# Optimization experiments

Hardware: AMD Instinct MI355X
Metric: run time of the kernel (lower is better)

The kernel has to match this reference:

```python
import jax, jax.numpy as jnp
import numpy as np

H = 1024      # hidden_size
NH = 16       # num_attention_heads
HD = H // NH  # head_size
DF = 4096     # ff intermediate
EPS = 1e-5


def layer_norm(x, g, b):
    mu = jnp.mean(x, axis=-1, keepdims=True)
    var = jnp.var(x, axis=-1, keepdims=True)
    return (x - mu) * jax.lax.rsqrt(var + EPS) * g + b


def setup_inputs() -> dict:
    key = jax.random.key(0)
    ks = jax.random.split(key, 4)
    s = 0.02
    return {
        "x": jax.random.normal(ks[0], (2, 2048, H), dtype=jnp.float32),
        "w_qkv": jax.random.normal(ks[1], (H, 3 * H), dtype=jnp.float32) * s,
        "ln1_g": jnp.ones((H,), jnp.float32),
        "ln1_b": jnp.zeros((H,), jnp.float32),
        "w1": jax.random.normal(ks[2], (H, DF), dtype=jnp.float32) * s,
        "b1": jnp.zeros((DF,), jnp.float32),
        "w2": jax.random.normal(ks[3], (DF, H), dtype=jnp.float32) * s,
        "b2": jnp.zeros((H,), jnp.float32),
        "ln2_g": jnp.ones((H,), jnp.float32),
        "ln2_b": jnp.zeros((H,), jnp.float32),
    }


def reference(x, w_qkv, ln1_g, ln1_b, w1, b1, w2, b2, ln2_g, ln2_b):
    b, s, h = x.shape
    # --- MHSelfAttention (naive) ---
    qkv = x @ w_qkv                                   # [b, s, 3h]
    qkv = qkv.reshape(b, s, 3, NH, HD)
    q, k, v = (jnp.moveaxis(qkv, 2, 0)                # [3, b, s, nh, hd]
               .transpose(0, 1, 3, 2, 4))             # [3, b, nh, s, hd]
    # NOTE: faithful quirk — scaled by sqrt(hidden_size), not head_size
    scores = jnp.einsum('bnqd,bnkd->bnqk', q, k) / jnp.sqrt(jnp.float32(h))
    probs = jax.nn.softmax(scores, axis=-1)
    ctx = jnp.einsum('bnqk,bnkd->bnqd', probs, v)     # [b, nh, s, hd]
    attn_out = ctx.transpose(0, 2, 1, 3).reshape(b, s, h)
    # post-norm residual (dropout = identity in eval)
    x = x + layer_norm(attn_out, ln1_g, ln1_b)
    # --- FFN ---
    ff = jax.nn.relu(x @ w1 + b1) @ w2 + b2
    x = x + layer_norm(ff, ln2_g, ln2_b)
    return x
```

## Files before the change

kernel.cpp:

```cpp
#include <hip/hip_runtime.h>


typedef unsigned short u16;
typedef unsigned int u32;
typedef __bf16 bf16x8 __attribute__((ext_vector_type(8)));
typedef float f32x4 __attribute__((ext_vector_type(4)));
typedef float f32x16 __attribute__((ext_vector_type(16)));
typedef u32 u32x4 __attribute__((ext_vector_type(4)));
typedef u16 u16x4 __attribute__((ext_vector_type(4)));

__device__ __forceinline__ u16 f2b(float f) {
  u32 u = __builtin_bit_cast(u32, f);
  u += 0x7fffu + ((u >> 16) & 1u);
  return (u16)(u >> 16);
}
__device__ __forceinline__ float b2f(u16 u) {
  return __builtin_bit_cast(float, (u32)u << 16);
}

__device__ __forceinline__ u32 cvtpk(float lo, float hi) {
  u32 r;
  asm("v_cvt_pk_bf16_f32 %0, %1, %2" : "=v"(r) : "v"(lo), "v"(hi));
  return r;
}

__device__ __forceinline__ void gld_lds16(const u16* g, u16* l) {
  __builtin_amdgcn_global_load_lds(
      (const __attribute__((address_space(1))) u32*)g,
      (__attribute__((address_space(3))) u32*)l, 16, 0, 0);
}

__global__ __launch_bounds__(256) void convert_bf16_kernel(
    const float* __restrict__ in, u16* __restrict__ out) {
  const int idx = blockIdx.x * 256 + threadIdx.x;
  float4 v = ((const float4*)in)[idx];
  u16x4 o = { f2b(v.x), f2b(v.y), f2b(v.z), f2b(v.w) };
  ((u16x4*)out)[idx] = o;
}

__global__ __launch_bounds__(256) void transpose_bf16_kernel(
    const float* __restrict__ in, u16* __restrict__ out, int R, int C) {
  __shared__ float tile[32][33];
  const int cb = blockIdx.x * 32, rb = blockIdx.y * 32;
  const int c = threadIdx.x & 31;
  const int r0 = threadIdx.x >> 5;
#pragma unroll
  for (int rr = 0; rr < 32; rr += 8)
    tile[r0 + rr][c] = in[(size_t)(rb + r0 + rr) * C + cb + c];
  __syncthreads();
#pragma unroll
  for (int rr = 0; rr < 32; rr += 8)
    out[(size_t)(cb + r0 + rr) * R + rb + c] = f2b(tile[c][r0 + rr]);
}

__global__ __launch_bounds__(256) void transpose_v_kernel(
    const u16* __restrict__ qkv, u16* __restrict__ vt) {
  __shared__ u16 t[64][70];
  const int bh = blockIdx.x, st = blockIdx.y;
  const int b = bh >> 4, nh = bh & 15;
  const int s0 = st * 64;
  const int r = threadIdx.x >> 3, c = (threadIdx.x & 7) << 3;
  const u16* src = qkv + (size_t)(b * 2048 + s0) * 3072 + 2048 + nh * 64;
#pragma unroll
  for (int rr = 0; rr < 64; rr += 32)
    *(u32x4*)&t[r + rr][c] = *(const u32x4*)(src + (size_t)(r + rr) * 3072 + c);
  __syncthreads();
  u16* dst = vt + ((size_t)bh * 64) * 2048 + s0;
#pragma unroll
  for (int rr = 0; rr < 64; rr += 32) {
    const int d = r + rr;
    u16 tmp[8];
#pragma unroll
    for (int j = 0; j < 8; ++j) tmp[j] = t[c + j][d];
    *(u32x4*)(dst + (size_t)d * 2048 + c) = *(u32x4*)tmp;
  }
}

#define GTILE(T, BUF, T2, VM)                                                 \
  {                                                                           \
    const u16(*Ab)[32] = As[BUF];                                             \
    const u16(*Bb)[32] = Bs[BUF];                                             \
    bf16x8 af[4], bf[4];                                                      \
    _Pragma("unroll") for (int nr = 0; nr < 4; ++nr)                          \
        bf[nr] = *(const bf16x8*)&Bb[wn * 64 + nr * 16 + l16][cRd];           \
    _Pragma("unroll") for (int mr = 0; mr < 4; ++mr)                          \
        af[mr] = *(const bf16x8*)&Ab[wm * 128 + mr * 16 + l16][cRd];          \
    if ((T2) >= 0) {                                                          \
      gld_lds16(Ag + (size_t)(T2) * 32,         &As[(T2) & 3][w * 16][0]);    \
      gld_lds16(Ag + rstep + (size_t)(T2) * 32, &As[(T2) & 3][128 + w * 16][0]);\
    }                                                                         \
    __builtin_amdgcn_sched_barrier(0);                                        \
    __builtin_amdgcn_s_barrier();                                             \
    asm volatile("s_waitcnt lgkmcnt(0)" ::: "memory");                        \
    __builtin_amdgcn_sched_barrier(0);                                        \
    __builtin_amdgcn_s_setprio(1);                                            \
    _Pragma("unroll") for (int mr = 0; mr < 4; ++mr)                          \
        _Pragma("unroll") for (int nr = 0; nr < 4; ++nr)                      \
            acc[mr][nr] = __builtin_amdgcn_mfma_f32_16x16x32_bf16(            \
                af[mr], bf[nr], acc[mr][nr], 0, 0, 0);                        \
    __builtin_amdgcn_s_setprio(0);                                            \
    __builtin_amdgcn_s_barrier();                                             \
    _Pragma("unroll") for (int mr = 0; mr < 4; ++mr)                          \
        af[mr] = *(const bf16x8*)&Ab[wm * 128 + 64 + mr * 16 + l16][cRd];     \
    if ((T2) >= 0) {                                                          \
      gld_lds16(Bg + (size_t)(T2) * 32,         &Bs[(T2) & 3][w * 16][0]);    \
      gld_lds16(Bg + rstep + (size_t)(T2) * 32, &Bs[(T2) & 3][128 + w * 16][0]);\
    }                                                                         \
    __builtin_amdgcn_sched_barrier(0);                                        \
    __builtin_amdgcn_s_barrier();                                             \
    asm volatile("s_waitcnt lgkmcnt(0)" ::: "memory");                        \
    __builtin_amdgcn_sched_barrier(0);                                        \
    __builtin_amdgcn_s_setprio(1);                                            \
    _Pragma("unroll") for (int mr = 0; mr < 4; ++mr)                          \
        _Pragma("unroll") for (int nr = 0; nr < 4; ++nr)                      \
            acc[4 + mr][nr] = __builtin_amdgcn_mfma_f32_16x16x32_bf16(        \
                af[mr], bf[nr], acc[4 + mr][nr], 0, 0, 0);                    \
    __builtin_amdgcn_s_setprio(0);                                            \
    if ((VM) == 4) asm volatile("s_waitcnt vmcnt(4)" ::: "memory");           \
    else if ((VM) == 0) asm volatile("s_waitcnt vmcnt(0)" ::: "memory");      \
    __builtin_amdgcn_s_barrier();                                             \
  }

__global__ __launch_bounds__(512) void gemm256_kernel(
    const u16* __restrict__ A, const u16* __restrict__ Bt,
    const float* __restrict__ bias, u16* __restrict__ Cb,
    int M, int N, int K, int relu,
    u16* __restrict__ Cb1, u16* __restrict__ Cb2, u16* __restrict__ Cb3) {
  const int nN = N >> 8;
  const int lin = (blockIdx.x & 7) * ((int)gridDim.x >> 3) + (blockIdx.x >> 3);
  const int m0 = (lin / nN) << 8;
  const int n0 = (lin % nN) << 8;
  const int z = blockIdx.y;
  if (z == 1) Cb = Cb1; else if (z == 2) Cb = Cb2; else if (z == 3) Cb = Cb3;

  const int tid = threadIdx.x;
  const int w = tid >> 6, lane = tid & 63;
  const int quad = lane >> 4, l16 = lane & 15;
  const int wm = w >> 2, wn = w & 3;

  __shared__ u16 As[4][256][32];
  __shared__ u16 Bs[4][256][32];

  f32x4 acc[8][4];
#pragma unroll
  for (int i = 0; i < 8; ++i)
#pragma unroll
    for (int j = 0; j < 4; ++j) acc[i][j] = {0.f, 0.f, 0.f, 0.f};

  const int srow = lane >> 2;
  const int scol = (((lane & 3) ^ (srow & 3)) << 3);
  const u16* Ag = A + (size_t)(m0 + w * 16 + srow) * K + (size_t)z * 1024 + scol;
  const u16* Bg = Bt + (size_t)(n0 + w * 16 + srow) * K + (size_t)z * 1024 + scol;
  const size_t rstep = (size_t)128 * K;

  const int cRd = ((quad ^ (l16 & 3)) << 3);

  gld_lds16(Ag,              &As[0][w * 16][0]);
  gld_lds16(Ag + rstep,      &As[0][128 + w * 16][0]);
  gld_lds16(Bg,              &Bs[0][w * 16][0]);
  gld_lds16(Bg + rstep,      &Bs[0][128 + w * 16][0]);
  gld_lds16(Ag + 32,         &As[1][w * 16][0]);
  gld_lds16(Ag + rstep + 32, &As[1][128 + w * 16][0]);
  gld_lds16(Bg + 32,         &Bs[1][w * 16][0]);
  gld_lds16(Bg + rstep + 32, &Bs[1][128 + w * 16][0]);
  asm volatile("s_waitcnt vmcnt(4)" ::: "memory");
  __builtin_amdgcn_s_barrier();

  for (int tt = 0; tt < 7; ++tt) {
    const int t = tt * 4;
    GTILE(t + 0, 0, t + 2, 4)
    GTILE(t + 1, 1, t + 3, 4)
    GTILE(t + 2, 2, t + 4, 4)
    GTILE(t + 3, 3, t + 5, 4)
  }
  GTILE(28, 0, 30, 4)
  GTILE(29, 1, 31, 4)
  GTILE(30, 2, -1, 0)
  GTILE(31, 3, -1, -1)

#pragma unroll
  for (int mr = 0; mr < 8; ++mr) {
    const int row = m0 + wm * 128 + mr * 16 + quad * 4;
#pragma unroll
    for (int nr = 0; nr < 4; ++nr) {
      const int col = n0 + wn * 64 + nr * 16 + l16;
      const float bv = bias ? bias[col] : 0.f;
#pragma unroll
      for (int r = 0; r < 4; ++r) {
        float v = acc[mr][nr][r] + bv;
        if (relu) v = fmaxf(v, 0.f);
        Cb[(size_t)(row + r) * N + col] = f2b(v);
      }
    }
  }
}

__global__ __launch_bounds__(256, 4) void attn_kernel(
    const u16* __restrict__ qkv, const u16* __restrict__ vt,
    float* __restrict__ Op0, float* __restrict__ Op1,
    float* __restrict__ lpart) {
  const int bh = blockIdx.x;
  const int qt = blockIdx.y;
  const int kz = blockIdx.z;
  const int b = bh >> 4, nh = bh & 15;
  const int tid = threadIdx.x;
  const int w = tid >> 6, lane = tid & 63;
  const int l32 = lane & 31, hi = lane >> 5;
  const float c2 = 0.04508422f;

  __shared__ u16 KS[64][64];
  __shared__ u16 VS[64][64];

  const size_t rs = 3072;
  const u16* qbase = qkv + (size_t)b * 2048 * rs + nh * 64;
  const u16* kbase = qbase + 1024;
  const u16* vbase = vt + (size_t)bh * 64 * 2048;
  const int q0 = qt * 128;
  const int k0beg = kz * 1024;

  bf16x8 aq[4];
  {
    const u16* qrow = qbase + (size_t)(q0 + w * 32 + l32) * rs + hi * 8;
#pragma unroll
    for (int ds = 0; ds < 4; ++ds) {
      u32x4 v = *(const u32x4*)(qrow + ds * 16);
      u16 ti[8], to[8];
      *(u32x4*)ti = v;
#pragma unroll
      for (int j = 0; j < 8; ++j) to[j] = f2b(b2f(ti[j]) * c2);
      u32x4 pk = *(u32x4*)to;
      aq[ds] = __builtin_bit_cast(bf16x8, pk);
    }
  }

  f32x16 Oacc[2];
#pragma unroll
  for (int dn = 0; dn < 2; ++dn)
#pragma unroll
    for (int i = 0; i < 16; ++i) Oacc[dn][i] = 0.f;
  float ls[4] = {0.f, 0.f, 0.f, 0.f};

  const int srow = lane >> 3;
  const int scol = ((lane & 7) ^ srow) << 3;

#pragma unroll 1
  for (int t = 0; t < 16; ++t) {
    const int k0 = k0beg + t * 64;
    __syncthreads();
    gld_lds16(kbase + (size_t)(k0 + w * 16 + srow) * rs + scol,       &KS[w * 16][0]);
    gld_lds16(kbase + (size_t)(k0 + w * 16 + 8 + srow) * rs + scol,   &KS[w * 16 + 8][0]);
    gld_lds16(vbase + (size_t)(w * 16 + srow) * 2048 + k0 + scol,     &VS[w * 16][0]);
    gld_lds16(vbase + (size_t)(w * 16 + 8 + srow) * 2048 + k0 + scol, &VS[w * 16 + 8][0]);
    __syncthreads();

    f32x16 S[2];
#pragma unroll
    for (int jt = 0; jt < 2; ++jt)
#pragma unroll
      for (int i = 0; i < 16; ++i) S[jt][i] = 0.f;
#pragma unroll
    for (int jt = 0; jt < 2; ++jt) {
      const int krow = jt * 32 + l32;
#pragma unroll
      for (int ds = 0; ds < 4; ++ds) {
        bf16x8 kv = *(const bf16x8*)&KS[krow][((2 * ds + hi) ^ (krow & 7)) << 3];
        S[jt] = __builtin_amdgcn_mfma_f32_32x32x16_bf16(kv, aq[ds], S[jt], 0, 0, 0);
      }
    }

    bf16x8 pa[4];
#pragma unroll
    for (int jt = 0; jt < 2; ++jt) {
      float p[16];
#pragma unroll
      for (int r = 0; r < 16; ++r) {
        p[r] = exp2f(S[jt][r]);
        ls[r & 3] += p[r];
      }
#pragma unroll
      for (int bq = 0; bq < 2; ++bq) {
        u32 x0 = cvtpk(p[8 * bq + 0], p[8 * bq + 1]);
        u32 y0 = cvtpk(p[8 * bq + 4], p[8 * bq + 5]);
        u32 x1 = cvtpk(p[8 * bq + 2], p[8 * bq + 3]);
        u32 y1 = cvtpk(p[8 * bq + 6], p[8 * bq + 7]);
        asm("v_permlane32_swap_b32 %0, %1" : "+v"(x0), "+v"(y0));
        asm("v_permlane32_swap_b32 %0, %1" : "+v"(x1), "+v"(y1));
        u32x4 dw = {x0, x1, y0, y1};
        pa[2 * jt + bq] = __builtin_bit_cast(bf16x8, dw);
      }
    }

#pragma unroll
    for (int dn = 0; dn < 2; ++dn) {
      const int vrow = dn * 32 + l32;
#pragma unroll
      for (int ks = 0; ks < 4; ++ks) {
        bf16x8 vv = *(const bf16x8*)&VS[vrow][((2 * ks + hi) ^ (vrow & 7)) << 3];
        Oacc[dn] = __builtin_amdgcn_mfma_f32_32x32x16_bf16(pa[ks], vv, Oacc[dn], 0, 0, 0);
      }
    }
  }

  float lsum = (ls[0] + ls[1]) + (ls[2] + ls[3]);
  const float ltot = lsum + __shfl_xor(lsum, 32);

  float* opart = kz ? Op1 : Op0;
  float* obase = opart + (size_t)b * 2048 * 1024 + (size_t)nh * 64;
  float* lbase = lpart + (size_t)kz * 4096 * 16 + (size_t)b * 2048 * 16 + nh;
#pragma unroll
  for (int r = 0; r < 16; ++r) {
    const int qrow = q0 + w * 32 + (r & 3) + 8 * (r >> 2) + 4 * hi;
#pragma unroll
    for (int dn = 0; dn < 2; ++dn)
      obase[(size_t)qrow * 1024 + dn * 32 + l32] = Oacc[dn][r];
  }
  if (lane < 32) lbase[(size_t)(q0 + w * 32 + l32) * 16] = ltot;
}

__global__ __launch_bounds__(256) void ln_attn_kernel(
    const float* __restrict__ O0, const float* __restrict__ O1,
    const float* __restrict__ l0, const float* __restrict__ l1,
    const float* __restrict__ xres, const float* __restrict__ g,
    const float* __restrict__ bb, float* __restrict__ outf,
    u16* __restrict__ outb) {
  const int row = blockIdx.x;
  const int tid = threadIdx.x;
  const int w = tid >> 6, lane = tid & 63;
  const int head = tid >> 4;
  float4 a0 = ((const float4*)(O0 + (size_t)row * 1024))[tid];
  float4 a1 = ((const float4*)(O1 + (size_t)row * 1024))[tid];
  const float inv = 1.f / (l0[row * 16 + head] + l1[row * 16 + head]);
  float4 v;
  v.x = (a0.x + a1.x) * inv;
  v.y = (a0.y + a1.y) * inv;
  v.z = (a0.z + a1.z) * inv;
  v.w = (a0.w + a1.w) * inv;
  float s = v.x + v.y + v.z + v.w;
  float s2 = v.x * v.x + v.y * v.y + v.z * v.z + v.w * v.w;
#pragma unroll
  for (int off = 32; off > 0; off >>= 1) {
    s += __shfl_xor(s, off);
    s2 += __shfl_xor(s2, off);
  }
  __shared__ float red[8];
  if (lane == 0) { red[w] = s; red[4 + w] = s2; }
  __syncthreads();
  s = red[0] + red[1] + red[2] + red[3];
  s2 = red[4] + red[5] + red[6] + red[7];
  const float mu = s * (1.f / 1024.f);
  const float var = s2 * (1.f / 1024.f) - mu * mu;
  const float rstd = rsqrtf(var + 1e-5f);
  float4 xr = ((const float4*)(xres + (size_t)row * 1024))[tid];
  float4 gv = ((const float4*)g)[tid];
  float4 bv = ((const float4*)bb)[tid];
  float4 o;
  o.x = xr.x + (v.x - mu) * rstd * gv.x + bv.x;
  o.y = xr.y + (v.y - mu) * rstd * gv.y + bv.y;
  o.z = xr.z + (v.z - mu) * rstd * gv.z + bv.z;
  o.w = xr.w + (v.w - mu) * rstd * gv.w + bv.w;
  ((float4*)(outf + (size_t)row * 1024))[tid] = o;
  u16x4 ob = { f2b(o.x), f2b(o.y), f2b(o.z), f2b(o.w) };
  *(u16x4*)(outb + (size_t)row * 1024 + (size_t)tid * 4) = ob;
}

__global__ __launch_bounds__(256) void ln_ffn_kernel(
    const u16* __restrict__ p0, const u16* __restrict__ p1,
    const u16* __restrict__ p2, const u16* __restrict__ p3,
    const float* __restrict__ bias, const float* __restrict__ xres,
    const float* __restrict__ g, const float* __restrict__ bb,
    float* __restrict__ outf) {
  const int row = blockIdx.x;
  const int tid = threadIdx.x;
  const int w = tid >> 6, lane = tid & 63;
  u16x4 a0 = ((const u16x4*)(p0 + (size_t)row * 1024))[tid];
  u16x4 a1 = ((const u16x4*)(p1 + (size_t)row * 1024))[tid];
  u16x4 a2 = ((const u16x4*)(p2 + (size_t)row * 1024))[tid];
  u16x4 a3 = ((const u16x4*)(p3 + (size_t)row * 1024))[tid];
  float4 bv4 = ((const float4*)bias)[tid];
  float4 v;
  v.x = (b2f(a0[0]) + b2f(a1[0])) + (b2f(a2[0]) + b2f(a3[0])) + bv4.x;
  v.y = (b2f(a0[1]) + b2f(a1[1])) + (b2f(a2[1]) + b2f(a3[1])) + bv4.y;
  v.z = (b2f(a0[2]) + b2f(a1[2])) + (b2f(a2[2]) + b2f(a3[2])) + bv4.z;
  v.w = (b2f(a0[3]) + b2f(a1[3])) + (b2f(a2[3]) + b2f(a3[3])) + bv4.w;
  float s = v.x + v.y + v.z + v.w;
  float s2 = v.x * v.x + v.y * v.y + v.z * v.z + v.w * v.w;
#pragma unroll
  for (int off = 32; off > 0; off >>= 1) {
    s += __shfl_xor(s, off);
    s2 += __shfl_xor(s2, off);
  }
  __shared__ float red[8];
  if (lane == 0) { red[w] = s; red[4 + w] = s2; }
  __syncthreads();
  s = red[0] + red[1] + red[2] + red[3];
  s2 = red[4] + red[5] + red[6] + red[7];
  const float mu = s * (1.f / 1024.f);
  const float var = s2 * (1.f / 1024.f) - mu * mu;
  const float rstd = rsqrtf(var + 1e-5f);
  float4 xr = ((const float4*)(xres + (size_t)row * 1024))[tid];
  float4 gv = ((const float4*)g)[tid];
  float4 bv = ((const float4*)bb)[tid];
  float4 o;
  o.x = xr.x + (v.x - mu) * rstd * gv.x + bv.x;
  o.y = xr.y + (v.y - mu) * rstd * gv.y + bv.y;
  o.z = xr.z + (v.z - mu) * rstd * gv.z + bv.z;
  o.w = xr.w + (v.w - mu) * rstd * gv.w + bv.w;
  ((float4*)(outf + (size_t)row * 1024))[tid] = o;
}

extern "C" void kernel_launch(void* const* d_in, const int* in_sizes, int n_in,
                              void* d_out, int out_size, void* d_ws, size_t ws_size,
                              hipStream_t stream) {
  const float* x     = (const float*)d_in[0];
  const float* w_qkv = (const float*)d_in[1];
  const float* ln1_g = (const float*)d_in[2];
  const float* ln1_b = (const float*)d_in[3];
  const float* w1    = (const float*)d_in[4];
  const float* b1    = (const float*)d_in[5];
  const float* w2    = (const float*)d_in[6];
  const float* b2    = (const float*)d_in[7];
  const float* ln2_g = (const float*)d_in[8];
  const float* ln2_b = (const float*)d_in[9];
  float* out = (float*)d_out;
  char* ws = (char*)d_ws;

  u16*   xb    = (u16*)(ws + 0);
  u16*   wqkvT = (u16*)(ws + 8388608);
  u16*   qkvb  = (u16*)(ws + 31457280);
  u16*   vT    = (u16*)(ws + 56623104);
  float* Op0   = (float*)(ws + 0);
  float* Op1   = (float*)(ws + 73400320);
  float* lp    = (float*)(ws + 90177536);
  float* x1    = (float*)(ws + 31457280);
  u16*   x1b   = (u16*)(ws + 48234496);
  u16*   w1T   = (u16*)(ws + 14680064);
  u16*   w2T   = (u16*)(ws + 23068672);
  u16*   h1    = (u16*)(ws + 56623104);
  u16*   fp0   = (u16*)(ws + 0);
  u16*   fp1   = (u16*)(ws + 8388608);
  u16*   fp2   = (u16*)(ws + 48234496);
  u16*   fp3   = (u16*)(ws + 90177536);

  convert_bf16_kernel<<<4096, 256, 0, stream>>>(x, xb);
  transpose_bf16_kernel<<<dim3(96, 32), 256, 0, stream>>>(w_qkv, wqkvT, 1024, 3072);

  gemm256_kernel<<<dim3(192, 1), 512, 0, stream>>>(
      xb, wqkvT, nullptr, qkvb, 4096, 3072, 1024, 0,
      nullptr, nullptr, nullptr);
  transpose_v_kernel<<<dim3(32, 32), 256, 0, stream>>>(qkvb, vT);
  attn_kernel<<<dim3(32, 16, 2), 256, 0, stream>>>(qkvb, vT, Op0, Op1, lp);

  ln_attn_kernel<<<4096, 256, 0, stream>>>(
      Op0, Op1, lp, lp + 4096 * 16, x, ln1_g, ln1_b, x1, x1b);

  transpose_bf16_kernel<<<dim3(128, 32), 256, 0, stream>>>(w1, w1T, 1024, 4096);
  transpose_bf16_kernel<<<dim3(32, 128), 256, 0, stream>>>(w2, w2T, 4096, 1024);

  gemm256_kernel<<<dim3(256, 1), 512, 0, stream>>>(
      x1b, w1T, b1, h1, 4096, 4096, 1024, 1,
      nullptr, nullptr, nullptr);
  gemm256_kernel<<<dim3(64, 4), 512, 0, stream>>>(
      h1, w2T, nullptr, fp0, 4096, 1024, 4096, 0,
      fp1, fp2, fp3);

  ln_ffn_kernel<<<4096, 256, 0, stream>>>(
      fp0, fp1, fp2, fp3, b2, x1, ln2_g, ln2_b, out);
}
```

Baseline: 325.7 us.

## Use a 3-stage LDS ring in the GEMM with one barrier per K-tile

New measurement: 320.7 us. About the same (-1.5%).

```diff
diff --git a/kernel.cpp b/kernel.cpp
--- a/kernel.cpp
+++ b/kernel.cpp
@@ -76,49 +76,44 @@
   }
 }
 
-#define GTILE(T, BUF, T2, VM)                                                 \
+#define GT(BUF, SBUF, T2, VM)                                                 \
   {                                                                           \
     const u16(*Ab)[32] = As[BUF];                                             \
     const u16(*Bb)[32] = Bs[BUF];                                             \
-    bf16x8 af[4], bf[4];                                                      \
+    bf16x8 af[4], bfr[4];                                                     \
     _Pragma("unroll") for (int nr = 0; nr < 4; ++nr)                          \
-        bf[nr] = *(const bf16x8*)&Bb[wn * 64 + nr * 16 + l16][cRd];           \
+        bfr[nr] = *(const bf16x8*)&Bb[wn * 64 + nr * 16 + l16][cRd];          \
     _Pragma("unroll") for (int mr = 0; mr < 4; ++mr)                          \
         af[mr] = *(const bf16x8*)&Ab[wm * 128 + mr * 16 + l16][cRd];          \
     if ((T2) >= 0) {                                                          \
-      gld_lds16(Ag + (size_t)(T2) * 32,         &As[(T2) & 3][w * 16][0]);    \
-      gld_lds16(Ag + rstep + (size_t)(T2) * 32, &As[(T2) & 3][128 + w * 16][0]);\
+      gld_lds16(Ag + (size_t)(T2) * 32,         &As[SBUF][w * 16][0]);        \
+      gld_lds16(Ag + rstep + (size_t)(T2) * 32, &As[SBUF][128 + w * 16][0]);  \
     }                                                                         \
-    __builtin_amdgcn_sched_barrier(0);                                        \
-    __builtin_amdgcn_s_barrier();                                             \
     asm volatile("s_waitcnt lgkmcnt(0)" ::: "memory");                        \
     __builtin_amdgcn_sched_barrier(0);                                        \
     __builtin_amdgcn_s_setprio(1);                                            \
     _Pragma("unroll") for (int mr = 0; mr < 4; ++mr)                          \
         _Pragma("unroll") for (int nr = 0; nr < 4; ++nr)                      \
             acc[mr][nr] = __builtin_amdgcn_mfma_f32_16x16x32_bf16(            \
-                af[mr], bf[nr], acc[mr][nr], 0, 0, 0);                        \
+                af[mr], bfr[nr], acc[mr][nr], 0, 0, 0);                       \
     __builtin_amdgcn_s_setprio(0);                                            \
-    __builtin_amdgcn_s_barrier();                                             \
     _Pragma("unroll") for (int mr = 0; mr < 4; ++mr)                          \
         af[mr] = *(const bf16x8*)&Ab[wm * 128 + 64 + mr * 16 + l16][cRd];     \
     if ((T2) >= 0) {                                                          \
-      gld_lds16(Bg + (size_t)(T2) * 32,         &Bs[(T2) & 3][w * 16][0]);    \
-      gld_lds16(Bg + rstep + (size_t)(T2) * 32, &Bs[(T2) & 3][128 + w * 16][0]);\
+      gld_lds16(Bg + (size_t)(T2) * 32,         &Bs[SBUF][w * 16][0]);        \
+      gld_lds16(Bg + rstep + (size_t)(T2) * 32, &Bs[SBUF][128 + w * 16][0]);  \
     }                                                                         \
-    __builtin_amdgcn_sched_barrier(0);                                        \
-    __builtin_amdgcn_s_barrier();                                             \
     asm volatile("s_waitcnt lgkmcnt(0)" ::: "memory");                        \
     __builtin_amdgcn_sched_barrier(0);                                        \
     __builtin_amdgcn_s_setprio(1);                                            \
     _Pragma("unroll") for (int mr = 0; mr < 4; ++mr)                          \
         _Pragma("unroll") for (int nr = 0; nr < 4; ++nr)                      \
             acc[4 + mr][nr] = __builtin_amdgcn_mfma_f32_16x16x32_bf16(        \
-                af[mr], bf[nr], acc[4 + mr][nr], 0, 0, 0);                    \
+                af[mr], bfr[nr], acc[4 + mr][nr], 0, 0, 0);                   \
     __builtin_amdgcn_s_setprio(0);                                            \
     if ((VM) == 4) asm volatile("s_waitcnt vmcnt(4)" ::: "memory");           \
     else if ((VM) == 0) asm volatile("s_waitcnt vmcnt(0)" ::: "memory");      \
-    __builtin_amdgcn_s_barrier();                                             \
+    if ((VM) >= 0) __builtin_amdgcn_s_barrier();                              \
   }
 
 __global__ __launch_bounds__(512) void gemm256_kernel(
@@ -138,8 +133,8 @@
   const int quad = lane >> 4, l16 = lane & 15;
   const int wm = w >> 2, wn = w & 3;
 
-  __shared__ u16 As[4][256][32];
-  __shared__ u16 Bs[4][256][32];
+  __shared__ u16 As[3][256][32];
+  __shared__ u16 Bs[3][256][32];
 
   f32x4 acc[8][4];
 #pragma unroll
@@ -166,17 +161,14 @@
   asm volatile("s_waitcnt vmcnt(4)" ::: "memory");
   __builtin_amdgcn_s_barrier();
 
-  for (int tt = 0; tt < 7; ++tt) {
-    const int t = tt * 4;
-    GTILE(t + 0, 0, t + 2, 4)
-    GTILE(t + 1, 1, t + 3, 4)
-    GTILE(t + 2, 2, t + 4, 4)
-    GTILE(t + 3, 3, t + 5, 4)
-  }
-  GTILE(28, 0, 30, 4)
-  GTILE(29, 1, 31, 4)
-  GTILE(30, 2, -1, 0)
-  GTILE(31, 3, -1, -1)
+  for (int tt = 0; tt < 10; ++tt) {
+    const int t = tt * 3;
+    GT(0, 2, t + 2, 4)
+    GT(1, 0, t + 3, 4)
+    GT(2, 1, t + 4, 4)
+  }
+  GT(0, 0, -1, 0)
+  GT(1, 0, -1, -1)
 
 #pragma unroll
   for (int mr = 0; mr < 8; ++mr) {
```
